# Performance work log

Hardware: AMD Instinct MI355X
Metric: run time of the kernel (lower is better)

## Reference

```python
import jax, jax.numpy as jnp
import numpy as np

B, SEQ, I_TSIZE, H, N_LAYERS = 512, 256, 64, 512, 2
E_CONST = 2.7183


def setup_inputs() -> dict:
    key = jax.random.key(0)
    ks = jax.random.split(key, 16)
    feats = jax.random.normal(ks[0], (B, SEQ, I_TSIZE - 1), dtype=jnp.float32)
    dt = jax.random.uniform(ks[1], (B, SEQ, 1), dtype=jnp.float32)  # elapsed time >= 0
    inputs_t = jnp.concatenate([feats, dt], axis=-1)  # [B, SEQ, I_TSIZE]
    i_size = I_TSIZE - 1
    inp = {"inputs_t": inputs_t}
    in_dims = [i_size, H]
    for l in range(N_LAYERS):
        c_inp = in_dims[l]
        s = 1.0 / np.sqrt(c_inp + H)
        inp[f"W{l}"] = jax.random.normal(ks[2 + 4 * l], (4 * H, c_inp + H), dtype=jnp.float32) * s
        inp[f"b{l}"] = jax.random.normal(ks[3 + 4 * l], (4 * H,), dtype=jnp.float32) * s
        sd = 1.0 / np.sqrt(H)
        inp[f"Wd{l}"] = jax.random.normal(ks[4 + 4 * l], (H, H), dtype=jnp.float32) * sd
        inp[f"bd{l}"] = jax.random.normal(ks[5 + 4 * l], (H,), dtype=jnp.float32) * sd
    return inp


def _tlstm_layer(curr_inp, W, b, Wd, bd):
    # curr_inp: [B, SEQ, feat+1] (last channel = dt). Scan over REVERSED time,
    # as in the torch loop `for t_seq in reversed(range(seq_l))`.
    batch = curr_inp.shape[0]
    h0 = jnp.zeros((batch, H), dtype=curr_inp.dtype)
    c0 = jnp.zeros((batch, H), dtype=curr_inp.dtype)

    def step(carry, xt):
        h, c = carry
        x, dt = xt[:, :-1], xt[:, -1:]
        T = 1.0 / jnp.log(dt + E_CONST)          # [B,1], broadcasts over H
        C_ST = jnp.tanh(h @ Wd.T + bd)
        h = h - C_ST + T * C_ST                  # time-decay correction
        z = jnp.concatenate([x, h], axis=1) @ W.T + b  # [B, 4H]
        ci, cf, co, cg = jnp.split(z, 4, axis=1)
        c_next = jax.nn.sigmoid(cf) * c + jax.nn.sigmoid(ci) * jnp.tanh(cg)
        h_next = jax.nn.sigmoid(co) * jnp.tanh(c_next)
        return (h_next, c_next), h_next

    xs = jnp.swapaxes(curr_inp[:, ::-1, :], 0, 1)  # [SEQ, B, feat+1], reversed time
    (h, c), hs = jax.lax.scan(step, (h0, c0), xs)
    # hs is in reversed-time order, matching torch's stack of output_inner
    layer_out = jnp.swapaxes(hs, 0, 1)  # [B, SEQ, H]
    return h, layer_out


def reference(inputs_t, W0, b0, Wd0, bd0, W1, b1, Wd1, bd1):
    t = inputs_t[..., -1:]  # [B, SEQ, 1], forward time order (as in torch code)
    params = [(W0, b0, Wd0, bd0), (W1, b1, Wd1, bd1)]
    curr = inputs_t
    h = None
    for (W, b, Wd, bd) in params:
        h, layer_out = _tlstm_layer(curr, W, b, Wd, bd)
        # NOTE: layer_out is in reversed time order but t is forward order;
        # this faithfully reproduces the original module's concatenation.
        curr = jnp.concatenate([layer_out, t], axis=-1)
    return h
```

## Files before the change

kernel.cpp:

```cpp
#include <hip/hip_runtime.h>
#include <stdint.h>

#define B_    512
#define SEQ_  256
#define H_    512
#define NSEQH (SEQ_ * H_)
#define NBLK  256
#define NTHR  (NBLK * 256)

using f32x4 = __attribute__((ext_vector_type(4))) float;
using s16x8 = __attribute__((ext_vector_type(8))) short;

#define WAITVM(N) asm volatile("s_waitcnt vmcnt(" #N ")" ::: "memory")
#define SBAR()    asm volatile("s_barrier" ::: "memory")

__device__ inline unsigned short f2bf(float f) {
  union { float f; uint32_t u; } x; x.f = f;
  uint32_t u = x.u;
  uint32_t r = u + 0x7fffu + ((u >> 16) & 1u);
  return (unsigned short)(r >> 16);
}
__device__ inline float bf2f(unsigned short h) {
  union { float f; uint32_t u; } x; x.u = ((uint32_t)h) << 16;
  return x.f;
}
__device__ inline float h2f(unsigned short u) {
  _Float16 h; __builtin_memcpy(&h, &u, 2); return (float)h;
}
__device__ inline unsigned short f2h(float f) {
  _Float16 h = (_Float16)f; unsigned short u; __builtin_memcpy(&u, &h, 2); return u;
}
__device__ inline float sigf(float x) { return 1.0f / (1.0f + expf(-x)); }

__device__ inline void gload16(const void* g, void* l) {
  __builtin_amdgcn_global_load_lds(
      (const __attribute__((address_space(1))) void*)g,
      (__attribute__((address_space(3))) void*)l, 16, 0, 0);
}
__device__ inline void gload16c(const void* g, void* l) {
  __builtin_amdgcn_global_load_lds(
      (const __attribute__((address_space(1))) void*)g,
      (__attribute__((address_space(3))) void*)l, 16, 0, 17);
}

__device__ __forceinline__ unsigned short ldh_coh(const unsigned short* p) {
  return __hip_atomic_load(p, __ATOMIC_RELAXED, __HIP_MEMORY_SCOPE_SYSTEM);
}
__device__ __forceinline__ void sth_coh(short* p, unsigned short v) {
  __hip_atomic_store((unsigned short*)p, v, __ATOMIC_RELAXED, __HIP_MEMORY_SCOPE_SYSTEM);
}

__device__ __forceinline__ void gbar_heavy(unsigned* bar) {
  __syncthreads();
  if (threadIdx.x == 0) {
    unsigned g = __hip_atomic_load(bar + 1, __ATOMIC_RELAXED, __HIP_MEMORY_SCOPE_AGENT);
    unsigned a = __hip_atomic_fetch_add(bar, 1u, __ATOMIC_ACQ_REL, __HIP_MEMORY_SCOPE_AGENT);
    if (a == (unsigned)(NBLK - 1)) {
      __hip_atomic_store(bar, 0u, __ATOMIC_RELAXED, __HIP_MEMORY_SCOPE_AGENT);
      __hip_atomic_store(bar + 1, g + 1u, __ATOMIC_RELEASE, __HIP_MEMORY_SCOPE_AGENT);
    } else {
      while (__hip_atomic_load(bar + 1, __ATOMIC_ACQUIRE, __HIP_MEMORY_SCOPE_AGENT) == g)
        __builtin_amdgcn_s_sleep(2);
    }
  }
  __syncthreads();
}

__device__ __forceinline__ void lbar(unsigned* bar, int& nb) {
  __syncthreads();
  ++nb;
  if (threadIdx.x == 0) {
    unsigned* leaf = bar + 32 + (blockIdx.x >> 5) * 32;
    unsigned* root = bar + 8;
    unsigned old = __hip_atomic_fetch_add(leaf, 1u, __ATOMIC_RELAXED, __HIP_MEMORY_SCOPE_SYSTEM);
    if ((old & 31u) == 31u)
      __hip_atomic_fetch_add(root, 1u, __ATOMIC_RELAXED, __HIP_MEMORY_SCOPE_SYSTEM);
    const unsigned target = (unsigned)(8 * nb);
    while ((int)(__hip_atomic_load(root, __ATOMIC_RELAXED, __HIP_MEMORY_SCOPE_SYSTEM) - target) < 0)
      __builtin_amdgcn_s_sleep(1);
  }
  __syncthreads();
}

__global__ void fill_kernel(float* __restrict__ out, int n, float v) {
  int i = blockIdx.x * blockDim.x + threadIdx.x;
  if (i < n) out[i] = v;
}

__device__ int compute_slot(const int* xcdmap, int myblk) {
  int cnt[8] = {0,0,0,0,0,0,0,0};
  int rank = -1;
  for (int b = 0; b < NBLK; ++b) {
    int x = xcdmap[b] & 7;
    int r = cnt[x]++;
    if (b == myblk) rank = r;
  }
  int myx = xcdmap[myblk] & 7;
  if (rank < 32) return myx * 32 + rank;
  int spill_idx = 0;
  {
    int c2[8] = {0,0,0,0,0,0,0,0};
    for (int b = 0; b < myblk; ++b) {
      int x = xcdmap[b] & 7;
      if (c2[x]++ >= 32) ++spill_idx;
    }
  }
  int k = 0;
  for (int g = 0; g < 8; ++g) {
    int filled = cnt[g] < 32 ? cnt[g] : 32;
    for (int rr = filled; rr < 32; ++rr) {
      if (k == spill_idx) return g * 32 + rr;
      ++k;
    }
  }
  return 0;
}

template<bool CVT>
__device__ __forceinline__ void g1_phase(
    char* LDS, int m0, int n0,
    const short* hhi, const short* hlo,
    const short* Wds, const float* bd, const float* tm1,
    short* huhi, short* hulo,
    const unsigned short* lo0_t, short* xhhi, short* xhlo)
{
  const int tid = threadIdx.x;
  const int w = tid >> 6, l = tid & 63;
  const int sr = tid >> 3;
  const int scs = (tid & 7) ^ (sr & 7);

  auto stage = [&](int kt) {
    char* base = LDS + (kt & 3) * 16384;
    const int kb = kt << 6;
    const size_t aoff = (size_t)(m0 + sr) * H_ + kb + scs * 8;
    gload16c(hhi + aoff, base + w * 1024);
    gload16c(hlo + aoff, base + 4096 + w * 1024);
    const size_t boff = (size_t)(n0 + sr) * 1024 + kb + scs * 8;
    gload16(Wds + boff,       base + 8192  + w * 1024);
    gload16(Wds + boff + 512, base + 12288 + w * 1024);
  };

  stage(0); stage(1); stage(2);

  const int wm = w & 1, wn = w >> 1;
  const int ar = wm * 16 + (l & 15);
  const int br = wn * 16 + (l & 15);
  const int koff = (l >> 4) * 16;
  const int aswz = (ar & 7) << 4;
  const int bswz = (br & 7) << 4;

  f32x4 acc = {0.f, 0.f, 0.f, 0.f};

  for (int kt = 0; kt < 8; ++kt) {
    if (kt < 6)       WAITVM(8);
    else if (kt == 6) WAITVM(4);
    else              WAITVM(0);
    SBAR();
    if (kt + 3 < 8) stage(kt + 3);
    char* base = LDS + (kt & 3) * 16384;
#pragma unroll
    for (int k2 = 0; k2 < 2; ++k2) {
      const int ao = (ar * 128 + k2 * 64 + koff) ^ aswz;
      const int bo = (br * 128 + k2 * 64 + koff) ^ bswz;
      s16x8 a_hi = *(const s16x8*)(base + ao);
      s16x8 a_lo = *(const s16x8*)(base + 4096 + ao);
      s16x8 b_hi = *(const s16x8*)(base + 8192 + bo);
      s16x8 b_lo = *(const s16x8*)(base + 12288 + bo);
      acc = __builtin_amdgcn_mfma_f32_16x16x32_bf16(a_hi, b_hi, acc, 0, 0, 0);
      acc = __builtin_amdgcn_mfma_f32_16x16x32_bf16(a_lo, b_hi, acc, 0, 0, 0);
      acc = __builtin_amdgcn_mfma_f32_16x16x32_bf16(a_hi, b_lo, acc, 0, 0, 0);
    }
  }

  const int n_abs = n0 + wn * 16 + (l & 15);
  const int mbase = m0 + wm * 16 + (l >> 4) * 4;
  const float bv = bd[n_abs];
#pragma unroll
  for (int r = 0; r < 4; ++r) {
    const int m_abs = mbase + r;
    const size_t off = (size_t)m_abs * H_ + n_abs;
    float cst = tanhf(acc[r] + bv);
    float hv = bf2f(ldh_coh((const unsigned short*)hhi + off)) +
               bf2f(ldh_coh((const unsigned short*)hlo + off));
    float hu = hv + tm1[m_abs] * cst;
    unsigned short hi = f2bf(hu);
    sth_coh(huhi + off, hi);
    sth_coh(hulo + off, f2bf(hu - bf2f(hi)));
    if (CVT) {
      float xv = h2f(ldh_coh(lo0_t + (size_t)m_abs * NSEQH + n_abs));
      unsigned short xh = f2bf(xv);
      sth_coh(xhhi + off, xh);
      sth_coh(xhlo + off, f2bf(xv - bf2f(xh)));
    }
  }
}

template<int K, int XK, int XSTR, bool STORE_LO0, bool XCOH>
__device__ __forceinline__ void g2_phase(
    char* LDS, int m0, int j0,
    const short* xhi, const short* xlo,
    const short* huhi, const short* hulo,
    const short* Wsp, const float* bias,
    f32x4& cv, short* hhi, short* hlo,
    unsigned short* lo0_t)
{
  constexpr int NT = K / 64;
  constexpr int KPS = 2 * K;
  const int tid = threadIdx.x;
  const int w = tid >> 6, l = tid & 63;

  auto stage = [&](int kt) {
    char* base = LDS + (kt & 1) * 32768;
    const int kb = kt << 6;
#pragma unroll
    for (int j = 0; j < 2; ++j) {
      const int s = tid + j * 256;
      const int r = s >> 3;
      const int cs = (s & 7) ^ (r & 7);
      const int dst = j * 4096 + w * 1024;
      if (kb < XK) {
        const size_t aoff = (size_t)(m0 + r) * XSTR + kb + cs * 8;
        if (XCOH) { gload16c(xhi + aoff, base + dst); gload16c(xlo + aoff, base + 8192 + dst); }
        else      { gload16 (xhi + aoff, base + dst); gload16 (xlo + aoff, base + 8192 + dst); }
      } else {
        const size_t aoff = (size_t)(m0 + r) * H_ + (kb - XK) + cs * 8;
        gload16c(huhi + aoff, base + dst);
        gload16c(hulo + aoff, base + 8192 + dst);
      }
      const int src_n = (r >> 4) * H_ + j0 + (r & 15);
      const size_t boff = (size_t)src_n * KPS + kb + cs * 8;
      gload16(Wsp + boff,     base + 16384 + dst);
      gload16(Wsp + boff + K, base + 24576 + dst);
    }
  };

  stage(0); stage(1);

  const int ar = w * 16 + (l & 15);
  const int koff = (l >> 4) * 16;
  const int aswz = (ar & 7) << 4;

  f32x4 acc[4];
#pragma unroll
  for (int i = 0; i < 4; ++i) acc[i] = (f32x4){0.f, 0.f, 0.f, 0.f};

  for (int kt = 0; kt < NT; ++kt) {
    if (kt + 1 < NT) WAITVM(8);
    else             WAITVM(0);
    SBAR();
    char* base = LDS + (kt & 1) * 32768;
#pragma unroll
    for (int k2 = 0; k2 < 2; ++k2) {
      const int ao = (ar * 128 + k2 * 64 + koff) ^ aswz;
      s16x8 a_hi = *(const s16x8*)(base + ao);
      s16x8 a_lo = *(const s16x8*)(base + 8192 + ao);
#pragma unroll
      for (int nf = 0; nf < 4; ++nf) {
        const int br = nf * 16 + (l & 15);
        const int bo = (br * 128 + k2 * 64 + koff) ^ ((br & 7) << 4);
        s16x8 b_hi = *(const s16x8*)(base + 16384 + bo);
        s16x8 b_lo = *(const s16x8*)(base + 24576 + bo);
        acc[nf] = __builtin_amdgcn_mfma_f32_16x16x32_bf16(a_hi, b_hi, acc[nf], 0, 0, 0);
        acc[nf] = __builtin_amdgcn_mfma_f32_16x16x32_bf16(a_lo, b_hi, acc[nf], 0, 0, 0);
        acc[nf] = __builtin_amdgcn_mfma_f32_16x16x32_bf16(a_hi, b_lo, acc[nf], 0, 0, 0);
      }
    }
    SBAR();
    if (kt + 2 < NT) stage(kt + 2);
  }

  const int j_abs = j0 + (l & 15);
  const float bi  = bias[j_abs];
  const float bfv = bias[H_ + j_abs];
  const float bo  = bias[2 * H_ + j_abs];
  const float bg  = bias[3 * H_ + j_abs];
  const int mbase = m0 + w * 16 + (l >> 4) * 4;
#pragma unroll
  for (int r = 0; r < 4; ++r) {
    const int m_abs = mbase + r;
    float zi = acc[0][r] + bi;
    float zf = acc[1][r] + bfv;
    float zo = acc[2][r] + bo;
    float zg = acc[3][r] + bg;
    float cn = sigf(zf) * cv[r] + sigf(zi) * tanhf(zg);
    float hn = sigf(zo) * tanhf(cn);
    cv[r] = cn;
    const size_t off = (size_t)m_abs * H_ + j_abs;
    unsigned short hi = f2bf(hn);
    sth_coh(hhi + off, hi);
    sth_coh(hlo + off, f2bf(hn - bf2f(hi)));
    if (STORE_LO0)
      sth_coh((short*)(lo0_t + (size_t)m_abs * NSEQH + j_abs), f2h(hn));
  }
}

__global__ __launch_bounds__(256, 1) void persist(
    const float* inputs,
    const float* W0, const float* b0, const float* Wd0, const float* bd0,
    const float* W1, const float* b1, const float* Wd1, const float* bd1,
    float* out,
    unsigned short* lo0, short* xinhi, short* xinlo,
    short* hhi, short* hlo, short* huhi, short* hulo,
    short* xhhi, short* xhlo,
    float* Tm1T, short* Wd0s, short* Wd1s, short* W0s, short* W1s,
    unsigned* bar, int* xcdmap)
{
  __shared__ __align__(16) char LDS[65536];
  const int gtid = blockIdx.x * 256 + threadIdx.x;
  int nb = 0;

  if (threadIdx.x == 0) {
    unsigned xcc;
    asm volatile("s_getreg_b32 %0, hwreg(20, 0, 32)" : "=s"(xcc));
    xcdmap[blockIdx.x] = (int)(xcc & 7u);
  }

  auto dosplit = [&](const float* W, short* Ws, int N, int Ksrc, int Kpad, int pad_at) {
    const int total = N * Kpad;
    for (int idx = gtid; idx < total; idx += NTHR) {
      int n = idx / Kpad, c = idx - n * Kpad;
      int sc = c;
      if (pad_at >= 0) { if (c == pad_at) sc = -1; else if (c > pad_at) sc = c - 1; }
      float v = 0.f;
      if (sc >= 0 && sc < Ksrc) v = W[(size_t)n * Ksrc + sc];
      unsigned short hi = f2bf(v);
      unsigned short lo = f2bf(v - bf2f(hi));
      size_t base = (size_t)n * (2 * Kpad);
      Ws[base + c]        = (short)hi;
      Ws[base + Kpad + c] = (short)lo;
    }
  };
  dosplit(Wd0, Wd0s, 512, 512, 512, -1);
  dosplit(Wd1, Wd1s, 512, 512, 512, -1);
  dosplit(W0, W0s, 2048, 575, 576, 63);
  dosplit(W1, W1s, 2048, 1024, 1024, -1);
  for (int idx = gtid; idx < B_ * SEQ_ * 64; idx += NTHR) {
    float v = inputs[idx];
    unsigned short hi = f2bf(v);
    xinhi[idx] = (short)hi;
    xinlo[idx] = (short)f2bf(v - bf2f(hi));
  }
  for (int idx = gtid; idx < B_ * SEQ_; idx += NTHR) {
    int b = idx / SEQ_, t = idx - b * SEQ_;
    float dt = inputs[(size_t)b * (SEQ_ * 64) + t * 64 + 63];
    Tm1T[t * B_ + b] = 1.0f / logf(dt + 2.7183f) - 1.0f;
  }
  for (int idx = gtid; idx < B_ * H_; idx += NTHR) {
    hhi[idx] = 0; hlo[idx] = 0;
  }
  gbar_heavy(bar);

  const int myw = compute_slot(xcdmap, blockIdx.x);
  const int wg = myw >> 5, rr = myw & 31;
  const int g1_n0 = (wg * 2 + (rr & 1)) * 32;
  const int g1_m0 = (rr >> 1) * 32;
  const int g2_j0 = (wg * 4 + (rr & 3)) * 16;
  const int g2_m0 = (rr >> 2) * 64;

  for (int layer = 0; layer < 2; ++layer) {
    f32x4 cv = {0.f, 0.f, 0.f, 0.f};
    if (layer == 1) {
      for (int idx = gtid; idx < B_ * H_; idx += NTHR) {
        sth_coh(hhi + idx, 0); sth_coh(hlo + idx, 0);
      }
      lbar(bar, nb);
    }
    for (int s = 0; s < SEQ_; ++s) {
      const int torig = SEQ_ - 1 - s;
      if (layer == 0) {
        g1_phase<false>(LDS, g1_m0, g1_n0, hhi, hlo, Wd0s, bd0,
                        Tm1T + (size_t)torig * B_, huhi, hulo,
                        nullptr, nullptr, nullptr);
        lbar(bar, nb);
        g2_phase<576, 64, SEQ_ * 64, true, false>(
            LDS, g2_m0, g2_j0,
            xinhi + (size_t)torig * 64, xinlo + (size_t)torig * 64,
            huhi, hulo, W0s, b0, cv, hhi, hlo,
            lo0 + (size_t)s * H_);
        lbar(bar, nb);
      } else {
        g1_phase<true>(LDS, g1_m0, g1_n0, hhi, hlo, Wd1s, bd1,
                       Tm1T + (size_t)torig * B_, huhi, hulo,
                       lo0 + (size_t)torig * H_, xhhi, xhlo);
        lbar(bar, nb);
        g2_phase<1024, 512, H_, false, true>(
            LDS, g2_m0, g2_j0,
            xhhi, xhlo, huhi, hulo, W1s, b1,
            cv, hhi, hlo, nullptr);
        lbar(bar, nb);
      }
    }
  }

  for (int idx = gtid; idx < B_ * H_; idx += NTHR)
    out[idx] = bf2f(ldh_coh((const unsigned short*)hhi + idx)) +
               bf2f(ldh_coh((const unsigned short*)hlo + idx));
}

extern "C" void kernel_launch(void* const* d_in, const int* in_sizes, int n_in,
                              void* d_out, int out_size, void* d_ws, size_t ws_size,
                              hipStream_t stream) {
  const float* inputs = (const float*)d_in[0];
  const float* W0  = (const float*)d_in[1];
  const float* b0  = (const float*)d_in[2];
  const float* Wd0 = (const float*)d_in[3];
  const float* bd0 = (const float*)d_in[4];
  const float* W1  = (const float*)d_in[5];
  const float* b1  = (const float*)d_in[6];
  const float* Wd1 = (const float*)d_in[7];
  const float* bd1 = (const float*)d_in[8];

  char* ws = (char*)d_ws;
  size_t off = 0;
  auto alloc = [&](size_t bytes) -> char* {
    char* p = ws + off;
    off += (bytes + 1023) & ~(size_t)1023;
    return p;
  };
  unsigned* bar = (unsigned*)alloc(2048);
  int* xcdmap = (int*)alloc(NBLK * 4);
  unsigned short* lo0 = (unsigned short*)alloc((size_t)B_ * SEQ_ * H_ * 2);
  short* xinhi = (short*)alloc((size_t)B_ * SEQ_ * 64 * 2);
  short* xinlo = (short*)alloc((size_t)B_ * SEQ_ * 64 * 2);
  short* hhi   = (short*)alloc((size_t)B_ * H_ * 2);
  short* hlo   = (short*)alloc((size_t)B_ * H_ * 2);
  short* huhi  = (short*)alloc((size_t)B_ * H_ * 2);
  short* hulo  = (short*)alloc((size_t)B_ * H_ * 2);
  short* xhhi  = (short*)alloc((size_t)B_ * H_ * 2);
  short* xhlo  = (short*)alloc((size_t)B_ * H_ * 2);
  float* Tm1T  = (float*)alloc((size_t)SEQ_ * B_ * 4);
  short* Wd0s  = (short*)alloc((size_t)512 * 1024 * 2);
  short* Wd1s  = (short*)alloc((size_t)512 * 1024 * 2);
  short* W0s   = (short*)alloc((size_t)2048 * 1152 * 2);
  short* W1s   = (short*)alloc((size_t)2048 * 2048 * 2);

  if (off > ws_size) {
    fill_kernel<<<(out_size + 255) / 256, 256, 0, stream>>>(
        (float*)d_out, out_size, (float)(ws_size >> 20));
    return;
  }

  hipMemsetAsync(bar, 0, 2048, stream);
  persist<<<NBLK, 256, 0, stream>>>(
      inputs, W0, b0, Wd0, bd0, W1, b1, Wd1, bd1,
      (float*)d_out,
      lo0, xinhi, xinlo,
      hhi, hlo, huhi, hulo, xhhi, xhlo,
      Tm1T, Wd0s, Wd1s, W0s, W1s, bar, xcdmap);
}
```

Measured before the change: 10.31 ms.

## Replace grid-wide tree barriers with per-batch-tile counter flags

Swaps the all-block hierarchical barrier used between the hidden-update and gate phases for monotonic counter flags scoped to each 64-row batch tile. Each tile has 32 blocks, and those blocks exchange only their own rows' h and hu, so tiles can drift apart instead of waiting on the whole grid every half-step. The layer-1 h reset and the final output copy become tile-local as well. The gate-phase LDS staging is moved to a separate 64KB region, doubling static LDS to 128KB, so it does not alias the first phase's buffers. This leans on the row-to-tile mapping being exactly consistent across phases, and on enough LDS being available.

```diff
diff --git a/kernel.cpp b/kernel.cpp
--- a/kernel.cpp
+++ b/kernel.cpp
@@ -66,17 +66,15 @@
   __syncthreads();
 }
 
-__device__ __forceinline__ void lbar(unsigned* bar, int& nb) {
+__device__ __forceinline__ void flag_signal(unsigned* f) {
+  WAITVM(0);
   __syncthreads();
-  ++nb;
-  if (threadIdx.x == 0) {
-    unsigned* leaf = bar + 32 + (blockIdx.x >> 5) * 32;
-    unsigned* root = bar + 8;
-    unsigned old = __hip_atomic_fetch_add(leaf, 1u, __ATOMIC_RELAXED, __HIP_MEMORY_SCOPE_SYSTEM);
-    if ((old & 31u) == 31u)
-      __hip_atomic_fetch_add(root, 1u, __ATOMIC_RELAXED, __HIP_MEMORY_SCOPE_SYSTEM);
-    const unsigned target = (unsigned)(8 * nb);
-    while ((int)(__hip_atomic_load(root, __ATOMIC_RELAXED, __HIP_MEMORY_SCOPE_SYSTEM) - target) < 0)
+  if (threadIdx.x == 0)
+    __hip_atomic_fetch_add(f, 1u, __ATOMIC_RELAXED, __HIP_MEMORY_SCOPE_SYSTEM);
+}
+__device__ __forceinline__ void flag_wait(unsigned* f, unsigned target) {
+  if (threadIdx.x == 0 && target) {
+    while (__hip_atomic_load(f, __ATOMIC_RELAXED, __HIP_MEMORY_SCOPE_SYSTEM) < target)
       __builtin_amdgcn_s_sleep(1);
   }
   __syncthreads();
@@ -210,35 +208,36 @@
   const int w = tid >> 6, l = tid & 63;
 
   auto stage = [&](int kt) {
-    char* base = LDS + (kt & 1) * 32768;
+    char* base = LDS + 65536 + (kt & 1) * 32768;
     const int kb = kt << 6;
 #pragma unroll
     for (int j = 0; j < 2; ++j) {
       const int s = tid + j * 256;
       const int r = s >> 3;
       const int cs = (s & 7) ^ (r & 7);
-      const int dst = j * 4096 + w * 1024;
+      char* dhi = base + j * 4096 + w * 1024;
+      char* dlo = base + 8192 + j * 4096 + w * 1024;
       if (kb < XK) {
         const size_t aoff = (size_t)(m0 + r) * XSTR + kb + cs * 8;
-        if (XCOH) { gload16c(xhi + aoff, base + dst); gload16c(xlo + aoff, base + 8192 + dst); }
-        else      { gload16 (xhi + aoff, base + dst); gload16 (xlo + aoff, base + 8192 + dst); }
+        if (XCOH) { gload16c(xhi + aoff, dhi); gload16c(xlo + aoff, dlo); }
+        else      { gload16 (xhi + aoff, dhi); gload16 (xlo + aoff, dlo); }
       } else {
         const size_t aoff = (size_t)(m0 + r) * H_ + (kb - XK) + cs * 8;
-        gload16c(huhi + aoff, base + dst);
-        gload16c(hulo + aoff, base + 8192 + dst);
+        gload16c(huhi + aoff, dhi);
+        gload16c(hulo + aoff, dlo);
       }
       const int src_n = (r >> 4) * H_ + j0 + (r & 15);
       const size_t boff = (size_t)src_n * KPS + kb + cs * 8;
-      gload16(Wsp + boff,     base + 16384 + dst);
-      gload16(Wsp + boff + K, base + 24576 + dst);
+      gload16(Wsp + boff,     base + 16384 + j * 4096 + w * 1024);
+      gload16(Wsp + boff + K, base + 24576 + j * 4096 + w * 1024);
     }
   };
 
   stage(0); stage(1);
 
   const int ar = w * 16 + (l & 15);
+  const int swz_a = (ar & 7) << 4;
   const int koff = (l >> 4) * 16;
-  const int aswz = (ar & 7) << 4;
 
   f32x4 acc[4];
 #pragma unroll
@@ -248,10 +247,10 @@
     if (kt + 1 < NT) WAITVM(8);
     else             WAITVM(0);
     SBAR();
-    char* base = LDS + (kt & 1) * 32768;
+    char* base = LDS + 65536 + (kt & 1) * 32768;
 #pragma unroll
     for (int k2 = 0; k2 < 2; ++k2) {
-      const int ao = (ar * 128 + k2 * 64 + koff) ^ aswz;
+      const int ao = (ar * 128 + k2 * 64 + koff) ^ swz_a;
       s16x8 a_hi = *(const s16x8*)(base + ao);
       s16x8 a_lo = *(const s16x8*)(base + 8192 + ao);
 #pragma unroll
@@ -305,9 +304,8 @@
     float* Tm1T, short* Wd0s, short* Wd1s, short* W0s, short* W1s,
     unsigned* bar, int* xcdmap)
 {
-  __shared__ __align__(16) char LDS[65536];
+  __shared__ __align__(16) char LDS[131072];
   const int gtid = blockIdx.x * 256 + threadIdx.x;
-  int nb = 0;
 
   if (threadIdx.x == 0) {
     unsigned xcc;
@@ -357,44 +355,59 @@
   const int g2_j0 = (wg * 4 + (rr & 3)) * 16;
   const int g2_m0 = (rr >> 2) * 64;
 
+  const int t = rr >> 2;
+  const int cid = wg * 4 + (rr & 3);
+  unsigned* g1d = bar + 512 + t * 32;
+  unsigned* g2d = bar + 768 + t * 32;
+  unsigned* zd  = bar + 256 + t * 32;
+
   for (int layer = 0; layer < 2; ++layer) {
     f32x4 cv = {0.f, 0.f, 0.f, 0.f};
     if (layer == 1) {
-      for (int idx = gtid; idx < B_ * H_; idx += NTHR) {
-        sth_coh(hhi + idx, 0); sth_coh(hlo + idx, 0);
+      flag_wait(g2d, 32u * SEQ_);
+      const size_t base = (size_t)t * 64 * H_;
+      for (int i = cid * 256 + threadIdx.x; i < 64 * H_; i += 32 * 256) {
+        sth_coh(hhi + base + i, 0); sth_coh(hlo + base + i, 0);
       }
-      lbar(bar, nb);
+      flag_signal(zd);
+      flag_wait(zd, 32u);
     }
     for (int s = 0; s < SEQ_; ++s) {
+      const unsigned ss = (unsigned)(layer * SEQ_ + s);
       const int torig = SEQ_ - 1 - s;
-      if (layer == 0) {
+      flag_wait(g2d, 32u * ss);
+      if (layer == 0)
         g1_phase<false>(LDS, g1_m0, g1_n0, hhi, hlo, Wd0s, bd0,
                         Tm1T + (size_t)torig * B_, huhi, hulo,
                         nullptr, nullptr, nullptr);
-        lbar(bar, nb);
+      else
+        g1_phase<true>(LDS, g1_m0, g1_n0, hhi, hlo, Wd1s, bd1,
+                       Tm1T + (size_t)torig * B_, huhi, hulo,
+                       lo0 + (size_t)torig * H_, xhhi, xhlo);
+      flag_signal(g1d);
+      flag_wait(g1d, 32u * (ss + 1));
+      if (layer == 0)
         g2_phase<576, 64, SEQ_ * 64, true, false>(
             LDS, g2_m0, g2_j0,
             xinhi + (size_t)torig * 64, xinlo + (size_t)torig * 64,
             huhi, hulo, W0s, b0, cv, hhi, hlo,
             lo0 + (size_t)s * H_);
-        lbar(bar, nb);
-      } else {
-        g1_phase<true>(LDS, g1_m0, g1_n0, hhi, hlo, Wd1s, bd1,
-                       Tm1T + (size_t)torig * B_, huhi, hulo,
-                       lo0 + (size_t)torig * H_, xhhi, xhlo);
-        lbar(bar, nb);
+      else
         g2_phase<1024, 512, H_, false, true>(
             LDS, g2_m0, g2_j0,
             xhhi, xhlo, huhi, hulo, W1s, b1,
             cv, hhi, hlo, nullptr);
-        lbar(bar, nb);
-      }
-    }
-  }
-
-  for (int idx = gtid; idx < B_ * H_; idx += NTHR)
-    out[idx] = bf2f(ldh_coh((const unsigned short*)hhi + idx)) +
-               bf2f(ldh_coh((const unsigned short*)hlo + idx));
+      flag_signal(g2d);
+    }
+  }
+
+  flag_wait(g2d, 32u * (unsigned)(2 * SEQ_));
+  {
+    const size_t base = (size_t)t * 64 * H_;
+    for (int i = cid * 256 + threadIdx.x; i < 64 * H_; i += 32 * 256)
+      out[base + i] = bf2f(ldh_coh((const unsigned short*)hhi + base + i)) +
+                      bf2f(ldh_coh((const unsigned short*)hlo + base + i));
+  }
 }
 
 extern "C" void kernel_launch(void* const* d_in, const int* in_sizes, int n_in,
@@ -417,7 +430,7 @@
     off += (bytes + 1023) & ~(size_t)1023;
     return p;
   };
-  unsigned* bar = (unsigned*)alloc(2048);
+  unsigned* bar = (unsigned*)alloc(4096);
   int* xcdmap = (int*)alloc(NBLK * 4);
   unsigned short* lo0 = (unsigned short*)alloc((size_t)B_ * SEQ_ * H_ * 2);
   short* xinhi = (short*)alloc((size_t)B_ * SEQ_ * 64 * 2);
@@ -440,7 +453,7 @@
     return;
   }
 
-  hipMemsetAsync(bar, 0, 2048, stream);
+  hipMemsetAsync(bar, 0, 4096, stream);
   persist<<<NBLK, 256, 0, stream>>>(
       inputs, W0, b0, Wd0, bd0, W1, b1, Wd1, bd1,
       (float*)d_out,
```

New measurement: 9.248 ms (median of 3 runs). 1.11x faster.
